# Optimization experiments

Measured on AMD Instinct MI355X. Metric: run time of the kernel, lower is better.

The kernel has to match this reference:

```python
import jax, jax.numpy as jnp
import numpy as np

N_HEAD = 16
VEC_DIM = 1024
KV_DIM = 64
SCALE = KV_DIM ** 0.5  # q is divided by sqrt(k_v_dim)

def gelu(x):
    # torch nn.GELU default = exact erf formulation
    return jax.nn.gelu(x, approximate=False)

def setup_inputs() -> dict:
    key = jax.random.key(0)
    ks = jax.random.split(key, 12)
    B, Sq, Sk = 2, 2048, 2048
    D, H = VEC_DIM, N_HEAD * KV_DIM
    s = lambda d: 1.0 / np.sqrt(d)
    return {
        "q_vec": jax.random.normal(ks[0], (B, Sq, D), jnp.float32),
        "k_vec": jax.random.normal(ks[1], (B, Sk, D), jnp.float32),
        # weights stored [in, out] so forward is x @ W
        "wq": jax.random.normal(ks[2], (D, H), jnp.float32) * s(D),
        "wk": jax.random.normal(ks[3], (D, H), jnp.float32) * s(D),
        "wv": jax.random.normal(ks[4], (D, H), jnp.float32) * s(D),
        "w_fc1": jax.random.normal(ks[5], (H, D), jnp.float32) * s(H),
        "w_m1": jax.random.normal(ks[6], (2 * D, D), jnp.float32) * s(2 * D),
        "b_m1": jnp.zeros((D,), jnp.float32),
        "w_m2": jax.random.normal(ks[7], (D, 2 * D), jnp.float32) * s(D),
        "b_m2": jnp.zeros((2 * D,), jnp.float32),
        "w_fc2": jax.random.normal(ks[8], (2 * D, D), jnp.float32) * s(2 * D),
    }

def reference(q_vec, k_vec, wq, wk, wv, w_fc1, w_m1, b_m1, w_m2, b_m2, w_fc2):
    B, Sq, D = q_vec.shape
    Sk = k_vec.shape[1]
    # QKV projections -> [B, H, S, dh]
    q = (q_vec @ wq).reshape(B, Sq, N_HEAD, KV_DIM).transpose(0, 2, 1, 3)
    k = (k_vec @ wk).reshape(B, Sk, N_HEAD, KV_DIM).transpose(0, 2, 1, 3)
    v = (k_vec @ wv).reshape(B, Sk, N_HEAD, KV_DIM).transpose(0, 2, 1, 3)
    # naive attention: full [B,H,Sq,Sk] score matrix (faithful to source)
    scores = jnp.einsum("bhqd,bhkd->bhqk", q / SCALE, k)
    attn = jax.nn.softmax(scores, axis=-1)
    q_out = jnp.einsum("bhqk,bhkd->bhqd", attn, v)
    q_out = q_out.transpose(0, 2, 1, 3).reshape(B, Sq, N_HEAD * KV_DIM)
    q_out = gelu(q_out @ w_fc1)  # fc1 (dropout is identity at p=0)
    x = jnp.concatenate((q_vec, q_out), axis=2)  # [B, Sq, 2D]
    # MLP with residual: Linear->GELU->Linear->GELU + x
    h = gelu(gelu(x @ w_m1 + b_m1) @ w_m2 + b_m2) + x
    out = gelu(h @ w_fc2)  # fc2
    return (out, attn)
```

## Files before the change

kernel.cpp:

```cpp
#include <hip/hip_runtime.h>
#include <cstdint>


typedef _Float16 half8 __attribute__((ext_vector_type(8)));
typedef float floatx4 __attribute__((ext_vector_type(4)));

__device__ __forceinline__ floatx4 mfma16(half8 a, half8 b, floatx4 c) {
    return __builtin_amdgcn_mfma_f32_16x16x32_f16(a, b, c, 0, 0, 0);
}

__device__ __forceinline__ float gelu_f(float x) {
    return 0.5f * x * (1.0f + erff(x * 0.70710678118654752f));
}

template <int ROWS, int ROWB>
__device__ __forceinline__ void stage_tile(char* lds, const _Float16* src, int ld) {
    constexpr int GPR = ROWB / 16;
    constexpr int ITERS = ROWS * GPR / 256;
    const int t = threadIdx.x;
#pragma unroll
    for (int i = 0; i < ITERS; i++) {
        const int id = i * 256 + t;
        const int r = id / GPR, g = id % GPR;
        float4 v = *(const float4*)(src + (size_t)r * ld + g * 8);
        *(float4*)(lds + r * ROWB + ((g * 16) ^ ((r & 7) << 4))) = v;
    }
}

__device__ __forceinline__ half8 frag(const char* lds, int row, int kbyte, int rowB) {
    return *(const half8*)(lds + row * rowB + (kbyte ^ ((row & 7) << 4)));
}


__global__ __launch_bounds__(256) void cvt_f32_f16(const float* __restrict__ src,
                                                   _Float16* __restrict__ dst, int n8) {
    int i = blockIdx.x * 256 + threadIdx.x;
    if (i < n8) {
        float4 a = ((const float4*)src)[i * 2];
        float4 b = ((const float4*)src)[i * 2 + 1];
        half8 h = {(_Float16)a.x, (_Float16)a.y, (_Float16)a.z, (_Float16)a.w,
                   (_Float16)b.x, (_Float16)b.y, (_Float16)b.z, (_Float16)b.w};
        ((half8*)dst)[i] = h;
    }
}

__global__ __launch_bounds__(256) void wtrans(const float* __restrict__ w,
                                              _Float16* __restrict__ wt, int K, int N) {
    __shared__ float tile[32][33];
    const int n0 = blockIdx.x * 32, k0 = blockIdx.y * 32;
    const int c = threadIdx.x & 31, r0 = threadIdx.x >> 5;
#pragma unroll
    for (int i = 0; i < 4; i++) {
        const int r = r0 + i * 8;
        tile[r][c] = w[(size_t)(k0 + r) * N + n0 + c];
    }
    __syncthreads();
#pragma unroll
    for (int i = 0; i < 4; i++) {
        const int r = r0 + i * 8;
        wt[(size_t)(n0 + r) * K + k0 + c] = (_Float16)tile[c][r];
    }
}


enum { E_QS = 0, E_KS = 1, E_VT = 2, E_GH = 3, E_BGH = 4, E_BGRH = 5, E_GF = 6 };

template <int EPI, bool CONCAT>
__global__ __launch_bounds__(256) void hgemm(
    int M, int N, int K,
    const _Float16* __restrict__ A, int lda, const _Float16* __restrict__ A2,
    const _Float16* __restrict__ B, int ldb,
    void* __restrict__ Cout, const float* __restrict__ bias,
    const float* __restrict__ resF, const _Float16* __restrict__ resH)
{
    __shared__ char ldsA[64 * 128];
    __shared__ char ldsB[128 * 128];
    const int t = threadIdx.x, l = t & 63, w = t >> 6;
    const int wm = w & 1, wn = w >> 1;
    const int lr = l & 15, lg = l >> 4;
    const int brow = blockIdx.y * 64, bcol = blockIdx.x * 128;

    floatx4 acc[2][4];
#pragma unroll
    for (int m = 0; m < 2; m++)
#pragma unroll
        for (int n = 0; n < 4; n++) acc[m][n] = (floatx4){0.f, 0.f, 0.f, 0.f};

    for (int k0 = 0; k0 < K; k0 += 64) {
        const _Float16* Ab = A;
        int kloc = k0;
        if constexpr (CONCAT) {
            if (k0 >= 1024) { Ab = A2; kloc = k0 - 1024; }
        }
        stage_tile<64, 128>(ldsA, Ab + (size_t)brow * lda + kloc, lda);
        stage_tile<128, 128>(ldsB, B + (size_t)bcol * ldb + k0, ldb);
        __syncthreads();
#pragma unroll
        for (int kk = 0; kk < 2; kk++) {
            const int kb = kk * 64 + lg * 16;
            half8 af[2], bf[4];
#pragma unroll
            for (int m = 0; m < 2; m++) af[m] = frag(ldsA, wm * 32 + m * 16 + lr, kb, 128);
#pragma unroll
            for (int n = 0; n < 4; n++) bf[n] = frag(ldsB, wn * 64 + n * 16 + lr, kb, 128);
#pragma unroll
            for (int m = 0; m < 2; m++)
#pragma unroll
                for (int n = 0; n < 4; n++)
                    acc[m][n] = mfma16(af[m], bf[n], acc[m][n]);
        }
        __syncthreads();
    }

#pragma unroll
    for (int m = 0; m < 2; m++)
#pragma unroll
        for (int n = 0; n < 4; n++)
#pragma unroll
            for (int r = 0; r < 4; r++) {
                const int grow = brow + wm * 32 + m * 16 + lg * 4 + r;
                const int gcol = bcol + wn * 64 + n * 16 + lr;
                float v = acc[m][n][r];
                if constexpr (EPI == E_QS) v *= 0.125f;
                if constexpr (EPI == E_QS || EPI == E_KS) {
                    const int bb = grow >> 11, s = grow & 2047;
                    const int hh = gcol >> 6, d = gcol & 63;
                    ((_Float16*)Cout)[(((size_t)(bb * 16 + hh) * 2048 + s) << 6) + d] =
                        (_Float16)v;
                } else if constexpr (EPI == E_VT) {
                    const int hh = grow >> 6, d = grow & 63;
                    const int bb = gcol >> 11, s = gcol & 2047;
                    ((_Float16*)Cout)[(((size_t)(bb * 16 + hh) * 64 + d) << 11) + s] =
                        (_Float16)v;
                } else if constexpr (EPI == E_GH) {
                    ((_Float16*)Cout)[(size_t)grow * N + gcol] = (_Float16)gelu_f(v);
                } else if constexpr (EPI == E_BGH) {
                    ((_Float16*)Cout)[(size_t)grow * N + gcol] =
                        (_Float16)gelu_f(v + bias[gcol]);
                } else if constexpr (EPI == E_BGRH) {
                    const float res = (gcol < 1024)
                        ? resF[(size_t)grow * 1024 + gcol]
                        : (float)resH[(size_t)grow * 1024 + (gcol - 1024)];
                    ((_Float16*)Cout)[(size_t)grow * N + gcol] =
                        (_Float16)(gelu_f(v + bias[gcol]) + res);
                } else {
                    ((float*)Cout)[(size_t)grow * N + gcol] = gelu_f(v);
                }
            }
}


__global__ __launch_bounds__(256) void attn_fused(
    const _Float16* __restrict__ Qh, const _Float16* __restrict__ Kh,
    const _Float16* __restrict__ Vh, float* __restrict__ attn,
    _Float16* __restrict__ QOh)
{
    __shared__ char ldsK[128 * 128];
    __shared__ char ldsV[64 * 256];
    __shared__ char ldsP[32 * 256];
    __shared__ float rsbuf[2][32];

    const int z = blockIdx.y;
    const int qs0 = blockIdx.x * 32;
    const int t = threadIdx.x, l = t & 63, w = t >> 6;
    const int wm = w & 1, wn = w >> 1;
    const int lr = l & 15, lg = l >> 4;

    const _Float16* Kz = Kh + (size_t)z * 2048 * 64;
    const _Float16* Vz = Vh + (size_t)z * 64 * 2048;

    half8 qf[2];
    {
        const _Float16* Qp =
            Qh + (size_t)z * 2048 * 64 + (size_t)(qs0 + wm * 16 + lr) * 64 + lg * 8;
        qf[0] = *(const half8*)(Qp);
        qf[1] = *(const half8*)(Qp + 32);
    }

    float rs[4] = {0.f, 0.f, 0.f, 0.f};
    for (int it = 0; it < 16; it++) {
        stage_tile<128, 128>(ldsK, Kz + (size_t)it * 128 * 64, 64);
        __syncthreads();
#pragma unroll
        for (int n16 = 0; n16 < 4; n16++) {
            floatx4 s = {0.f, 0.f, 0.f, 0.f};
#pragma unroll
            for (int kk = 0; kk < 2; kk++)
                s = mfma16(qf[kk],
                           frag(ldsK, wn * 64 + n16 * 16 + lr, kk * 64 + lg * 16, 128), s);
#pragma unroll
            for (int r = 0; r < 4; r++) rs[r] += __expf(s[r]);
        }
        __syncthreads();
    }
#pragma unroll
    for (int off = 1; off < 16; off <<= 1)
#pragma unroll
        for (int r = 0; r < 4; r++) rs[r] += __shfl_xor(rs[r], off);
    if (lr == 0)
#pragma unroll
        for (int r = 0; r < 4; r++) rsbuf[wn][wm * 16 + lg * 4 + r] = rs[r];
    __syncthreads();
    float rinv[4];
#pragma unroll
    for (int r = 0; r < 4; r++) {
        const int ridx = wm * 16 + lg * 4 + r;
        rinv[r] = 1.0f / (rsbuf[0][ridx] + rsbuf[1][ridx]);
    }

    float* attnz = attn + (size_t)z * 2048 * 2048;
    floatx4 o[2] = {{0.f, 0.f, 0.f, 0.f}, {0.f, 0.f, 0.f, 0.f}};
    for (int it = 0; it < 16; it++) {
        stage_tile<128, 128>(ldsK, Kz + (size_t)it * 128 * 64, 64);
        stage_tile<64, 256>(ldsV, Vz + it * 128, 2048);
        __syncthreads();
#pragma unroll
        for (int n16 = 0; n16 < 4; n16++) {
            floatx4 s = {0.f, 0.f, 0.f, 0.f};
#pragma unroll
            for (int kk = 0; kk < 2; kk++)
                s = mfma16(qf[kk],
                           frag(ldsK, wn * 64 + n16 * 16 + lr, kk * 64 + lg * 16, 128), s);
#pragma unroll
            for (int r = 0; r < 4; r++) {
                const float p = __expf(s[r]) * rinv[r];
                const int prow = wm * 16 + lg * 4 + r;
                const int pcol = wn * 64 + n16 * 16 + lr;
                attnz[(size_t)(qs0 + prow) * 2048 + it * 128 + pcol] = p;
                *(_Float16*)(ldsP + prow * 256 + ((pcol * 2) ^ ((prow & 7) << 4))) =
                    (_Float16)p;
            }
        }
        __syncthreads();
#pragma unroll
        for (int kb = 0; kb < 4; kb++) {
            half8 pf = frag(ldsP, wm * 16 + lr, kb * 64 + lg * 16, 256);
#pragma unroll
            for (int n16 = 0; n16 < 2; n16++) {
                half8 vf = frag(ldsV, wn * 32 + n16 * 16 + lr, kb * 64 + lg * 16, 256);
                o[n16] = mfma16(pf, vf, o[n16]);
            }
        }
        __syncthreads();
    }

    const int bb = z >> 4, hh = z & 15;
#pragma unroll
    for (int n16 = 0; n16 < 2; n16++)
#pragma unroll
        for (int r = 0; r < 4; r++) {
            const int row = qs0 + wm * 16 + lg * 4 + r;
            const int d = wn * 32 + n16 * 16 + lr;
            QOh[((size_t)bb * 2048 + row) * 1024 + hh * 64 + d] = (_Float16)o[n16][r];
        }
}


extern "C" void kernel_launch(void* const* d_in, const int* in_sizes, int n_in,
                              void* d_out, int out_size, void* d_ws, size_t ws_size,
                              hipStream_t stream)
{
    const float* q_vec = (const float*)d_in[0];
    const float* k_vec = (const float*)d_in[1];
    const float* wq    = (const float*)d_in[2];
    const float* wk    = (const float*)d_in[3];
    const float* wv    = (const float*)d_in[4];
    const float* w_fc1 = (const float*)d_in[5];
    const float* w_m1  = (const float*)d_in[6];
    const float* b_m1  = (const float*)d_in[7];
    const float* w_m2  = (const float*)d_in[8];
    const float* b_m2  = (const float*)d_in[9];
    const float* w_fc2 = (const float*)d_in[10];

    float* out  = (float*)d_out;
    float* attn = out + (size_t)2 * 2048 * 1024;

    _Float16* W = (_Float16*)d_ws;
    const size_t M1 = 1048576, M2 = 2097152, M4 = 4194304;
    _Float16* qvec_h = W;
    _Float16* kvec_h = W + M4;
    _Float16* WTq  = W + 2 * M4;
    _Float16* WTk  = WTq + M1;
    _Float16* WTv  = WTk + M1;
    _Float16* WTf1 = WTv + M1;
    _Float16* WTm1 = WTf1 + M1;
    _Float16* WTm2 = WTm1 + M2;
    _Float16* WTf2 = WTm2 + M2;
    _Float16* Qh   = WTf2 + M2;
    _Float16* Kh   = Qh + M4;
    _Float16* Vh   = Kh + M4;
    _Float16* QOh  = Vh + M4;
    _Float16* g1h  = Kh;
    _Float16* t1h  = Vh;
    _Float16* hh   = W;

    dim3 blk(256);

    cvt_f32_f16<<<dim3(2048), blk, 0, stream>>>(q_vec, qvec_h, 524288);
    cvt_f32_f16<<<dim3(2048), blk, 0, stream>>>(k_vec, kvec_h, 524288);
    wtrans<<<dim3(32, 32), blk, 0, stream>>>(wq, WTq, 1024, 1024);
    wtrans<<<dim3(32, 32), blk, 0, stream>>>(wk, WTk, 1024, 1024);
    wtrans<<<dim3(32, 32), blk, 0, stream>>>(wv, WTv, 1024, 1024);
    wtrans<<<dim3(32, 32), blk, 0, stream>>>(w_fc1, WTf1, 1024, 1024);
    wtrans<<<dim3(32, 64), blk, 0, stream>>>(w_m1, WTm1, 2048, 1024);
    wtrans<<<dim3(64, 32), blk, 0, stream>>>(w_m2, WTm2, 1024, 2048);
    wtrans<<<dim3(32, 64), blk, 0, stream>>>(w_fc2, WTf2, 2048, 1024);

    hgemm<E_QS, false><<<dim3(8, 64), blk, 0, stream>>>(
        4096, 1024, 1024, qvec_h, 1024, nullptr, WTq, 1024, Qh, nullptr, nullptr, nullptr);
    hgemm<E_KS, false><<<dim3(8, 64), blk, 0, stream>>>(
        4096, 1024, 1024, kvec_h, 1024, nullptr, WTk, 1024, Kh, nullptr, nullptr, nullptr);
    hgemm<E_VT, false><<<dim3(32, 16), blk, 0, stream>>>(
        1024, 4096, 1024, WTv, 1024, nullptr, kvec_h, 1024, Vh, nullptr, nullptr, nullptr);

    attn_fused<<<dim3(64, 32), blk, 0, stream>>>(Qh, Kh, Vh, attn, QOh);

    hgemm<E_GH, false><<<dim3(8, 64), blk, 0, stream>>>(
        4096, 1024, 1024, QOh, 1024, nullptr, WTf1, 1024, g1h, nullptr, nullptr, nullptr);
    hgemm<E_BGH, true><<<dim3(8, 64), blk, 0, stream>>>(
        4096, 1024, 2048, qvec_h, 1024, g1h, WTm1, 2048, t1h, b_m1, nullptr, nullptr);
    hgemm<E_BGRH, false><<<dim3(16, 64), blk, 0, stream>>>(
        4096, 2048, 1024, t1h, 1024, nullptr, WTm2, 1024, hh, b_m2, q_vec, g1h);
    hgemm<E_GF, false><<<dim3(8, 64), blk, 0, stream>>>(
        4096, 1024, 2048, hh, 2048, nullptr, WTf2, 2048, out, nullptr, nullptr, nullptr);
}
```

Baseline: 938.4 us.

## Use direct global-to-LDS loads, 128x128 GEMM tiles, coalesced attn stores

Tile staging now uses global_load_lds, which writes global data straight into LDS without passing through registers, with the XOR swizzle applied on the source side. The GEMM block tile grows from 64x128 to 128x128 and the attention block from 32 to 64 query rows, so each K/V tile loaded into LDS is reused more. The probability matrix is now written to global memory from the fp16 LDS copy as coalesced float4 stores instead of scattered scalar stores. The costs are fewer blocks per launch, more registers per thread, and attention probabilities that carry fp16 rounding in the fp32 output.

After: 0.9999 ms. +6.6%, slower.

```diff
diff --git a/kernel.cpp b/kernel.cpp
--- a/kernel.cpp
+++ b/kernel.cpp
@@ -13,22 +13,29 @@
     return 0.5f * x * (1.0f + erff(x * 0.70710678118654752f));
 }
 
-template <int ROWS, int ROWB>
-__device__ __forceinline__ void stage_tile(char* lds, const _Float16* src, int ld) {
-    constexpr int GPR = ROWB / 16;
-    constexpr int ITERS = ROWS * GPR / 256;
-    const int t = threadIdx.x;
-#pragma unroll
-    for (int i = 0; i < ITERS; i++) {
-        const int id = i * 256 + t;
-        const int r = id / GPR, g = id % GPR;
-        float4 v = *(const float4*)(src + (size_t)r * ld + g * 8);
-        *(float4*)(lds + r * ROWB + ((g * 16) ^ ((r & 7) << 4))) = v;
-    }
-}
-
-__device__ __forceinline__ half8 frag(const char* lds, int row, int kbyte, int rowB) {
-    return *(const half8*)(lds + row * rowB + (kbyte ^ ((row & 7) << 4)));
+__device__ __forceinline__ void gll16(const void* g, void* l) {
+    __builtin_amdgcn_global_load_lds(
+        (const __attribute__((address_space(1))) unsigned int*)g,
+        (__attribute__((address_space(3))) unsigned int*)l, 16, 0, 0);
+}
+
+template <int ROWS, int GPR>
+__device__ __forceinline__ void stage_gll(char* lds, const _Float16* src, int ld,
+                                          int w, int l) {
+    constexpr int PW = ROWS * GPR / 4;
+    constexpr int NI = PW / 64;
+#pragma unroll
+    for (int i = 0; i < NI; i++) {
+        const int idx = w * PW + i * 64 + l;
+        const int r = idx / GPR;
+        const int g = (idx % GPR) ^ (r & 7);
+        gll16(src + (size_t)r * ld + g * 8, lds + (w * PW + i * 64) * 16);
+    }
+}
+
+template <int ROWB>
+__device__ __forceinline__ half8 frag(const char* lds, int row, int kbyte) {
+    return *(const half8*)(lds + row * ROWB + (kbyte ^ ((row & 7) << 4)));
 }
 
 
@@ -73,16 +80,16 @@
     void* __restrict__ Cout, const float* __restrict__ bias,
     const float* __restrict__ resF, const _Float16* __restrict__ resH)
 {
-    __shared__ char ldsA[64 * 128];
+    __shared__ char ldsA[128 * 128];
     __shared__ char ldsB[128 * 128];
     const int t = threadIdx.x, l = t & 63, w = t >> 6;
     const int wm = w & 1, wn = w >> 1;
     const int lr = l & 15, lg = l >> 4;
-    const int brow = blockIdx.y * 64, bcol = blockIdx.x * 128;
-
-    floatx4 acc[2][4];
-#pragma unroll
-    for (int m = 0; m < 2; m++)
+    const int brow = blockIdx.y * 128, bcol = blockIdx.x * 128;
+
+    floatx4 acc[4][4];
+#pragma unroll
+    for (int m = 0; m < 4; m++)
 #pragma unroll
         for (int n = 0; n < 4; n++) acc[m][n] = (floatx4){0.f, 0.f, 0.f, 0.f};
 
@@ -92,19 +99,19 @@
         if constexpr (CONCAT) {
             if (k0 >= 1024) { Ab = A2; kloc = k0 - 1024; }
         }
-        stage_tile<64, 128>(ldsA, Ab + (size_t)brow * lda + kloc, lda);
-        stage_tile<128, 128>(ldsB, B + (size_t)bcol * ldb + k0, ldb);
+        stage_gll<128, 8>(ldsA, Ab + (size_t)brow * lda + kloc, lda, w, l);
+        stage_gll<128, 8>(ldsB, B + (size_t)bcol * ldb + k0, ldb, w, l);
         __syncthreads();
 #pragma unroll
         for (int kk = 0; kk < 2; kk++) {
             const int kb = kk * 64 + lg * 16;
-            half8 af[2], bf[4];
-#pragma unroll
-            for (int m = 0; m < 2; m++) af[m] = frag(ldsA, wm * 32 + m * 16 + lr, kb, 128);
-#pragma unroll
-            for (int n = 0; n < 4; n++) bf[n] = frag(ldsB, wn * 64 + n * 16 + lr, kb, 128);
-#pragma unroll
-            for (int m = 0; m < 2; m++)
+            half8 af[4], bf[4];
+#pragma unroll
+            for (int m = 0; m < 4; m++) af[m] = frag<128>(ldsA, wm * 64 + m * 16 + lr, kb);
+#pragma unroll
+            for (int n = 0; n < 4; n++) bf[n] = frag<128>(ldsB, wn * 64 + n * 16 + lr, kb);
+#pragma unroll
+            for (int m = 0; m < 4; m++)
 #pragma unroll
                 for (int n = 0; n < 4; n++)
                     acc[m][n] = mfma16(af[m], bf[n], acc[m][n]);
@@ -113,12 +120,12 @@
     }
 
 #pragma unroll
-    for (int m = 0; m < 2; m++)
+    for (int m = 0; m < 4; m++)
 #pragma unroll
         for (int n = 0; n < 4; n++)
 #pragma unroll
             for (int r = 0; r < 4; r++) {
-                const int grow = brow + wm * 32 + m * 16 + lg * 4 + r;
+                const int grow = brow + wm * 64 + m * 16 + lg * 4 + r;
                 const int gcol = bcol + wn * 64 + n * 16 + lr;
                 float v = acc[m][n][r];
                 if constexpr (EPI == E_QS) v *= 0.125f;
@@ -157,11 +164,11 @@
 {
     __shared__ char ldsK[128 * 128];
     __shared__ char ldsV[64 * 256];
-    __shared__ char ldsP[32 * 256];
-    __shared__ float rsbuf[2][32];
+    __shared__ char ldsP[64 * 256];
+    __shared__ float rsbuf[2][64];
 
     const int z = blockIdx.y;
-    const int qs0 = blockIdx.x * 32;
+    const int qs0 = blockIdx.x * 64;
     const int t = threadIdx.x, l = t & 63, w = t >> 6;
     const int wm = w & 1, wn = w >> 1;
     const int lr = l & 15, lg = l >> 4;
@@ -169,90 +176,130 @@
     const _Float16* Kz = Kh + (size_t)z * 2048 * 64;
     const _Float16* Vz = Vh + (size_t)z * 64 * 2048;
 
-    half8 qf[2];
+    half8 qf[2][2];
     {
         const _Float16* Qp =
-            Qh + (size_t)z * 2048 * 64 + (size_t)(qs0 + wm * 16 + lr) * 64 + lg * 8;
-        qf[0] = *(const half8*)(Qp);
-        qf[1] = *(const half8*)(Qp + 32);
-    }
-
-    float rs[4] = {0.f, 0.f, 0.f, 0.f};
+            Qh + (size_t)z * 2048 * 64 + (size_t)(qs0 + wm * 32 + lr) * 64 + lg * 8;
+#pragma unroll
+        for (int m = 0; m < 2; m++)
+#pragma unroll
+            for (int kk = 0; kk < 2; kk++)
+                qf[m][kk] = *(const half8*)(Qp + m * 16 * 64 + kk * 32);
+    }
+
+    float rs[2][4] = {};
     for (int it = 0; it < 16; it++) {
-        stage_tile<128, 128>(ldsK, Kz + (size_t)it * 128 * 64, 64);
-        __syncthreads();
-#pragma unroll
-        for (int n16 = 0; n16 < 4; n16++) {
-            floatx4 s = {0.f, 0.f, 0.f, 0.f};
+        stage_gll<128, 8>(ldsK, Kz + (size_t)it * 128 * 64, 64, w, l);
+        __syncthreads();
+        half8 kf[4][2];
+#pragma unroll
+        for (int n16 = 0; n16 < 4; n16++)
 #pragma unroll
             for (int kk = 0; kk < 2; kk++)
-                s = mfma16(qf[kk],
-                           frag(ldsK, wn * 64 + n16 * 16 + lr, kk * 64 + lg * 16, 128), s);
-#pragma unroll
-            for (int r = 0; r < 4; r++) rs[r] += __expf(s[r]);
-        }
+                kf[n16][kk] = frag<128>(ldsK, wn * 64 + n16 * 16 + lr, kk * 64 + lg * 16);
+#pragma unroll
+        for (int m = 0; m < 2; m++)
+#pragma unroll
+            for (int n16 = 0; n16 < 4; n16++) {
+                floatx4 s = {0.f, 0.f, 0.f, 0.f};
+#pragma unroll
+                for (int kk = 0; kk < 2; kk++) s = mfma16(qf[m][kk], kf[n16][kk], s);
+#pragma unroll
+                for (int r = 0; r < 4; r++) rs[m][r] += __expf(s[r]);
+            }
         __syncthreads();
     }
 #pragma unroll
     for (int off = 1; off < 16; off <<= 1)
 #pragma unroll
-        for (int r = 0; r < 4; r++) rs[r] += __shfl_xor(rs[r], off);
+        for (int m = 0; m < 2; m++)
+#pragma unroll
+            for (int r = 0; r < 4; r++) rs[m][r] += __shfl_xor(rs[m][r], off);
     if (lr == 0)
 #pragma unroll
-        for (int r = 0; r < 4; r++) rsbuf[wn][wm * 16 + lg * 4 + r] = rs[r];
+        for (int m = 0; m < 2; m++)
+#pragma unroll
+            for (int r = 0; r < 4; r++)
+                rsbuf[wn][wm * 32 + m * 16 + lg * 4 + r] = rs[m][r];
     __syncthreads();
-    float rinv[4];
-#pragma unroll
-    for (int r = 0; r < 4; r++) {
-        const int ridx = wm * 16 + lg * 4 + r;
-        rinv[r] = 1.0f / (rsbuf[0][ridx] + rsbuf[1][ridx]);
-    }
+    float rinv[2][4];
+#pragma unroll
+    for (int m = 0; m < 2; m++)
+#pragma unroll
+        for (int r = 0; r < 4; r++) {
+            const int row = wm * 32 + m * 16 + lg * 4 + r;
+            rinv[m][r] = 1.0f / (rsbuf[0][row] + rsbuf[1][row]);
+        }
+    __syncthreads();
 
     float* attnz = attn + (size_t)z * 2048 * 2048;
-    floatx4 o[2] = {{0.f, 0.f, 0.f, 0.f}, {0.f, 0.f, 0.f, 0.f}};
+    floatx4 o[2][2] = {{{0.f,0.f,0.f,0.f},{0.f,0.f,0.f,0.f}},
+                       {{0.f,0.f,0.f,0.f},{0.f,0.f,0.f,0.f}}};
     for (int it = 0; it < 16; it++) {
-        stage_tile<128, 128>(ldsK, Kz + (size_t)it * 128 * 64, 64);
-        stage_tile<64, 256>(ldsV, Vz + it * 128, 2048);
-        __syncthreads();
-#pragma unroll
-        for (int n16 = 0; n16 < 4; n16++) {
-            floatx4 s = {0.f, 0.f, 0.f, 0.f};
+        stage_gll<128, 8>(ldsK, Kz + (size_t)it * 128 * 64, 64, w, l);
+        stage_gll<64, 16>(ldsV, Vz + it * 128, 2048, w, l);
+        __syncthreads();
+        half8 kf[4][2];
+#pragma unroll
+        for (int n16 = 0; n16 < 4; n16++)
 #pragma unroll
             for (int kk = 0; kk < 2; kk++)
-                s = mfma16(qf[kk],
-                           frag(ldsK, wn * 64 + n16 * 16 + lr, kk * 64 + lg * 16, 128), s);
+                kf[n16][kk] = frag<128>(ldsK, wn * 64 + n16 * 16 + lr, kk * 64 + lg * 16);
+#pragma unroll
+        for (int m = 0; m < 2; m++)
+#pragma unroll
+            for (int n16 = 0; n16 < 4; n16++) {
+                floatx4 s = {0.f, 0.f, 0.f, 0.f};
+#pragma unroll
+                for (int kk = 0; kk < 2; kk++) s = mfma16(qf[m][kk], kf[n16][kk], s);
+#pragma unroll
+                for (int r = 0; r < 4; r++) {
+                    const float p = __expf(s[r]) * rinv[m][r];
+                    const int prow = wm * 32 + m * 16 + lg * 4 + r;
+                    const int pcol = wn * 64 + n16 * 16 + lr;
+                    *(_Float16*)(ldsP + prow * 256 + ((pcol * 2) ^ ((prow & 7) << 4))) =
+                        (_Float16)p;
+                }
+            }
+        __syncthreads();
+#pragma unroll
+        for (int i = 0; i < 4; i++) {
+            const int idx = i * 256 + t;
+            const int r = idx >> 4, g = idx & 15;
+            half8 ph = *(const half8*)(ldsP + r * 256 + ((g * 16) ^ ((r & 7) << 4)));
+            float* dst = attnz + (size_t)(qs0 + r) * 2048 + it * 128 + g * 8;
+            float4 lo = {(float)ph[0], (float)ph[1], (float)ph[2], (float)ph[3]};
+            float4 hi = {(float)ph[4], (float)ph[5], (float)ph[6], (float)ph[7]};
+            *(float4*)dst = lo;
+            *(float4*)(dst + 4) = hi;
+        }
+#pragma unroll
+        for (int kkv = 0; kkv < 4; kkv++) {
+            const int kb = kkv * 64 + lg * 16;
+            half8 pf[2], vf[2];
+#pragma unroll
+            for (int m = 0; m < 2; m++) pf[m] = frag<256>(ldsP, wm * 32 + m * 16 + lr, kb);
+#pragma unroll
+            for (int n = 0; n < 2; n++) vf[n] = frag<256>(ldsV, wn * 32 + n * 16 + lr, kb);
+#pragma unroll
+            for (int m = 0; m < 2; m++)
+#pragma unroll
+                for (int n = 0; n < 2; n++) o[m][n] = mfma16(pf[m], vf[n], o[m][n]);
+        }
+        __syncthreads();
+    }
+
+    const int bb = z >> 4, hh = z & 15;
+#pragma unroll
+    for (int m = 0; m < 2; m++)
+#pragma unroll
+        for (int n = 0; n < 2; n++)
 #pragma unroll
             for (int r = 0; r < 4; r++) {
-                const float p = __expf(s[r]) * rinv[r];
-                const int prow = wm * 16 + lg * 4 + r;
-                const int pcol = wn * 64 + n16 * 16 + lr;
-                attnz[(size_t)(qs0 + prow) * 2048 + it * 128 + pcol] = p;
-                *(_Float16*)(ldsP + prow * 256 + ((pcol * 2) ^ ((prow & 7) << 4))) =
-                    (_Float16)p;
+                const int row = qs0 + wm * 32 + m * 16 + lg * 4 + r;
+                const int d = wn * 32 + n * 16 + lr;
+                QOh[((size_t)bb * 2048 + row) * 1024 + hh * 64 + d] = (_Float16)o[m][n][r];
             }
-        }
-        __syncthreads();
-#pragma unroll
-        for (int kb = 0; kb < 4; kb++) {
-            half8 pf = frag(ldsP, wm * 16 + lr, kb * 64 + lg * 16, 256);
-#pragma unroll
-            for (int n16 = 0; n16 < 2; n16++) {
-                half8 vf = frag(ldsV, wn * 32 + n16 * 16 + lr, kb * 64 + lg * 16, 256);
-                o[n16] = mfma16(pf, vf, o[n16]);
-            }
-        }
-        __syncthreads();
-    }
-
-    const int bb = z >> 4, hh = z & 15;
-#pragma unroll
-    for (int n16 = 0; n16 < 2; n16++)
-#pragma unroll
-        for (int r = 0; r < 4; r++) {
-            const int row = qs0 + wm * 16 + lg * 4 + r;
-            const int d = wn * 32 + n16 * 16 + lr;
-            QOh[((size_t)bb * 2048 + row) * 1024 + hh * 64 + d] = (_Float16)o[n16][r];
-        }
 }
 
 
@@ -306,21 +353,21 @@
     wtrans<<<dim3(64, 32), blk, 0, stream>>>(w_m2, WTm2, 1024, 2048);
     wtrans<<<dim3(32, 64), blk, 0, stream>>>(w_fc2, WTf2, 2048, 1024);
 
-    hgemm<E_QS, false><<<dim3(8, 64), blk, 0, stream>>>(
+    hgemm<E_QS, false><<<dim3(8, 32), blk, 0, stream>>>(
         4096, 1024, 1024, qvec_h, 1024, nullptr, WTq, 1024, Qh, nullptr, nullptr, nullptr);
-    hgemm<E_KS, false><<<dim3(8, 64), blk, 0, stream>>>(
+    hgemm<E_KS, false><<<dim3(8, 32), blk, 0, stream>>>(
         4096, 1024, 1024, kvec_h, 1024, nullptr, WTk, 1024, Kh, nullptr, nullptr, nullptr);
-    hgemm<E_VT, false><<<dim3(32, 16), blk, 0, stream>>>(
+    hgemm<E_VT, false><<<dim3(32, 8), blk, 0, stream>>>(
         1024, 4096, 1024, WTv, 1024, nullptr, kvec_h, 1024, Vh, nullptr, nullptr, nullptr);
 
-    attn_fused<<<dim3(64, 32), blk, 0, stream>>>(Qh, Kh, Vh, attn, QOh);
-
-    hgemm<E_GH, false><<<dim3(8, 64), blk, 0, stream>>>(
+    attn_fused<<<dim3(32, 32), blk, 0, stream>>>(Qh, Kh, Vh, attn, QOh);
+
+    hgemm<E_GH, false><<<dim3(8, 32), blk, 0, stream>>>(
         4096, 1024, 1024, QOh, 1024, nullptr, WTf1, 1024, g1h, nullptr, nullptr, nullptr);
-    hgemm<E_BGH, true><<<dim3(8, 64), blk, 0, stream>>>(
+    hgemm<E_BGH, true><<<dim3(8, 32), blk, 0, stream>>>(
         4096, 1024, 2048, qvec_h, 1024, g1h, WTm1, 2048, t1h, b_m1, nullptr, nullptr);
-    hgemm<E_BGRH, false><<<dim3(16, 64), blk, 0, stream>>>(
+    hgemm<E_BGRH, false><<<dim3(16, 32), blk, 0, stream>>>(
         4096, 2048, 1024, t1h, 1024, nullptr, WTm2, 1024, hh, b_m2, q_vec, g1h);
-    hgemm<E_GF, false><<<dim3(8, 64), blk, 0, stream>>>(
+    hgemm<E_GF, false><<<dim3(8, 32), blk, 0, stream>>>(
         4096, 1024, 2048, hh, 2048, nullptr, WTf2, 2048, out, nullptr, nullptr, nullptr);
 }
```
